# Kernel tuning notes

Measured on AMD Instinct MI355X. Metric: run time of the kernel, lower is better.

The kernel has to match this reference:

```python
import jax, jax.numpy as jnp
import numpy as np
from jax import lax

ALIGNED_H = 7
ALIGNED_W = 7
SPATIAL_SCALE = 0.125
B, C, H, W = 4, 512, 96, 96
R = 512
IMG = 768  # image resolution (features are image/8)


def setup_inputs() -> dict:
    key = jax.random.key(0)
    k1, k2, k3, k4, k5, k6 = jax.random.split(key, 6)
    features = jax.random.normal(k1, (B, C, H, W), dtype=jnp.float32)
    # realistic rois: [batch_idx, x1, y1, x2, y2] in image coordinates
    bi = jax.random.randint(k2, (R,), 0, B).astype(jnp.float32)
    cx = jax.random.uniform(k3, (R,), minval=32.0, maxval=float(IMG - 32))
    cy = jax.random.uniform(k4, (R,), minval=32.0, maxval=float(IMG - 32))
    bw = jax.random.uniform(k5, (R,), minval=16.0, maxval=256.0)
    bh = jax.random.uniform(k6, (R,), minval=16.0, maxval=256.0)
    x1 = jnp.clip(cx - bw / 2, 0.0, IMG - 1.0)
    x2 = jnp.clip(cx + bw / 2, 0.0, IMG - 1.0)
    y1 = jnp.clip(cy - bh / 2, 0.0, IMG - 1.0)
    y2 = jnp.clip(cy + bh / 2, 0.0, IMG - 1.0)
    rois = jnp.stack([bi, x1, y1, x2, y2], axis=1)
    return {"features": features, "rois": rois}


def _roi_align_ada(features, rois, ah, aw, scale):
    """RoIAlignAda: per output pixel, average of a 3x3 adaptive-stride grid of
    bilinear samples centered at the bin point (RT-MDNet ROIAlignAdaForward)."""
    b, c, h, w = features.shape
    r = rois.shape[0]
    batch_ind = rois[:, 0].astype(jnp.int32)
    x1 = rois[:, 1] * scale
    y1 = rois[:, 2] * scale
    x2 = rois[:, 3] * scale
    y2 = rois[:, 4] * scale
    roi_w = jnp.maximum(x2 - x1, 0.0)
    roi_h = jnp.maximum(y2 - y1, 0.0)
    bin_h = roi_h / (ah - 1.0)  # [R]
    bin_w = roi_w / (aw - 1.0)
    ph = jnp.arange(ah, dtype=jnp.float32)
    pw = jnp.arange(aw, dtype=jnp.float32)
    hc = y1[:, None] + ph[None, :] * bin_h[:, None]  # [R, AH] bin centers
    wc = x1[:, None] + pw[None, :] * bin_w[:, None]  # [R, AW]
    stride_h = jnp.maximum(1.0, jnp.round(bin_h / 3.0))  # [R]
    stride_w = jnp.maximum(1.0, jnp.round(bin_w / 3.0))

    center_ok = ((hc >= 0) & (hc < h))[:, :, None] & ((wc >= 0) & (wc < w))[:, None, :]  # [R,AH,AW]

    # flatten spatial for gathers: [B*H*W, C]
    f = features.transpose(0, 2, 3, 1).reshape(b * h * w, c)
    base = batch_ind[:, None, None] * (h * w)  # [R,1,1]

    acc = jnp.zeros((r, ah, aw, c), dtype=features.dtype)
    cnt = jnp.zeros((r, ah, aw), dtype=features.dtype)
    for sh in (-1.0, 0.0, 1.0):
        for sw in (-1.0, 0.0, 1.0):
            ch = hc + sh * stride_h[:, None]  # [R,AH]
            cw = wc + sw * stride_w[:, None]  # [R,AW]
            valid = ((ch >= 0) & (ch < h))[:, :, None] & ((cw >= 0) & (cw < w))[:, None, :]
            hs = jnp.clip(jnp.floor(ch), 0.0, h - 2.0)
            ws = jnp.clip(jnp.floor(cw), 0.0, w - 2.0)
            hr = (ch - hs)[:, :, None]  # [R,AH,1]
            wr = (cw - ws)[:, None, :] * jnp.ones((r, ah, aw), features.dtype)[:, :1, :1]  # broadcast helper
            wr = (cw - ws)[:, None, :]  # [R,1,AW]
            hsi = hs.astype(jnp.int32)[:, :, None]  # [R,AH,1]
            wsi = ws.astype(jnp.int32)[:, None, :]  # [R,1,AW]
            ul = base + hsi * w + wsi  # [R,AH,AW]
            v = (f[ul] * ((1.0 - hr) * (1.0 - wr))[..., None]
                 + f[ul + 1] * ((1.0 - hr) * wr)[..., None]
                 + f[ul + w] * (hr * (1.0 - wr))[..., None]
                 + f[ul + w + 1] * (hr * wr)[..., None])  # [R,AH,AW,C]
            acc = acc + jnp.where(valid[..., None], v, 0.0)
            cnt = cnt + valid.astype(features.dtype)

    out = jnp.where(center_ok[..., None], acc / jnp.maximum(cnt, 1.0)[..., None], 0.0)
    return out.transpose(0, 3, 1, 2)  # [R, C, AH, AW]


def reference(features, rois):
    x = _roi_align_ada(features, rois, ALIGNED_H + 4, ALIGNED_W + 4, SPATIAL_SCALE)  # [R,C,11,11]
    # fused 3x3 stride-2 max pool -> [R, C, 5, 5]
    out = lax.reduce_window(x, -jnp.inf, lax.max,
                            window_dimensions=(1, 1, 3, 3),
                            window_strides=(1, 1, 2, 2),
                            padding='VALID')
    return out
```

## Files before the change

### kernel.cpp

```cpp
#include <hip/hip_runtime.h>
#include <stdint.h>

typedef unsigned short u16;
typedef unsigned int   u32;

#define Bn 4
#define Cc 512
#define Hh 96
#define Ww 96
#define HWc (Hh*Ww)
#define AH 11
#define Rr 512
#define CP (Cc/2)

__device__ __forceinline__ u16 f2bf(float f){
  u32 u = __float_as_uint(f);
  u += 0x7fffu + ((u>>16)&1u);
  return (u16)(u>>16);
}
__device__ __forceinline__ u32 pk2(float a, float b){
  return (u32)f2bf(a) | ((u32)f2bf(b)<<16);
}

__global__ __launch_bounds__(256)
void transpose_kernel(const float* __restrict__ in, u32* __restrict__ out){
  __shared__ u32 tile[128*64];
  const int t = threadIdx.x;
  const int hw0 = blockIdx.x*128, c0 = blockIdx.y*128, b = blockIdx.z;
  {
    const int q = t & 31, cp0 = t >> 5;
    const float* ib = in + ((size_t)(b*Cc + c0))*HWc + hw0 + 4*q;
    #pragma unroll
    for (int p=0;p<8;++p){
      const int cp = cp0 + p*8;
      const float* pa = ib + (size_t)(2*cp)*HWc;
      float4 A = *(const float4*)pa;
      float4 B = *(const float4*)(pa + HWc);
      const int cs = cp ^ q;
      tile[(4*q+0)*64 + cs] = pk2(A.x,B.x);
      tile[(4*q+1)*64 + cs] = pk2(A.y,B.y);
      tile[(4*q+2)*64 + cs] = pk2(A.z,B.z);
      tile[(4*q+3)*64 + cs] = pk2(A.w,B.w);
    }
  }
  __syncthreads();
  {
    const int l = t & 63, wv = t >> 6;
    u32* ob = out + ((size_t)b*HWc + hw0)*CP + (c0>>1) + l;
    #pragma unroll
    for (int k=0;k<32;++k){
      const int hw = wv*32 + k;
      ob[(size_t)hw*CP] = tile[hw*64 + (l ^ (hw>>2))];
    }
  }
}

__global__ __launch_bounds__(128)
void roi_align_max_nhwc(const u32* __restrict__ feat,
                        const float* __restrict__ rois,
                        float* __restrict__ out)
{
  __shared__ __align__(16) int4   s_ro[AH];
  __shared__ __align__(16) float4 s_rw[AH];
  __shared__ __align__(16) int4   s_co[AH];
  __shared__ __align__(16) float4 s_cw[AH];
  __shared__ int s_b;
  __shared__ __align__(16) float s_out[256*25];

  const int t    = threadIdx.x;
  const int r    = blockIdx.x >> 1;
  const int half = blockIdx.x & 1;

  if (t == 0){
    int b = (int)rois[r*5+0];
    s_b = min(max(b, 0), Bn-1);
  }

  if (t < AH || (t >= 64 && t < 64+AH)){
    const bool isrow = (t < AH);
    const int  p = isrow ? t : t-64;
    const float* rp = rois + r*5;
    const float c1 = rp[isrow?2:1], c2 = rp[isrow?4:3];
    float lo  = __fmul_rn(c1, 0.125f);
    float hi  = __fmul_rn(c2, 0.125f);
    float ext = fmaxf(__fsub_rn(hi,lo), 0.0f);
    float bin = __fdiv_rn(ext, 10.0f);
    float ctr = __fadd_rn(lo, __fmul_rn((float)p, bin));
    float strd = fmaxf(1.0f, rintf(__fdiv_rn(bin, 3.0f)));
    bool ok = (ctr >= 0.0f) && (ctr < 96.0f);
    int rws[6]; float wts[6]; int nv=0;
    #pragma unroll
    for (int s=0;s<3;++s){
      float cc = __fadd_rn(ctr, __fmul_rn((float)(s-1), strd));
      bool vv = (cc >= 0.0f) && (cc < 96.0f);
      float fl = fminf(fmaxf(floorf(cc),0.0f),94.0f);
      float fr = __fsub_rn(cc, fl);
      int ri = (int)fl;
      rws[2*s]=ri; rws[2*s+1]=ri+1;
      wts[2*s]  = vv ? __fsub_rn(1.0f,fr) : 0.0f;
      wts[2*s+1]= vv ? fr : 0.0f;
      nv += vv?1:0;
    }
    float sc = ok ? (1.0f/(float)nv) : 0.0f;
    int cr[4]={0,0,0,0}; float cwv[4]={0.0f,0.0f,0.0f,0.0f}; int n=0;
    for (int k=0;k<6;++k){
      float wk=wts[k]; if (wk==0.0f) continue;
      int rr=rws[k]; bool fnd=false;
      for (int j=0;j<n;++j) if (cr[j]==rr){ cwv[j]+=wk; fnd=true; break; }
      if (!fnd && n<4){ cr[n]=rr; cwv[n]=wk; ++n; }
    }
    const int mul = isrow ? (Ww*CP) : CP;
    if (isrow){
      s_ro[p] = make_int4(cr[0]*mul, cr[1]*mul, cr[2]*mul, cr[3]*mul);
      s_rw[p] = make_float4(cwv[0]*sc, cwv[1]*sc, cwv[2]*sc, cwv[3]*sc);
    } else {
      s_co[p] = make_int4(cr[0]*mul, cr[1]*mul, cr[2]*mul, cr[3]*mul);
      s_cw[p] = make_float4(cwv[0]*sc, cwv[1]*sc, cwv[2]*sc, cwv[3]*sc);
    }
  }
  __syncthreads();

  const u32* fbase = feat + (size_t)s_b*((size_t)HWc*CP);
  const int tb = half*128 + t;

  int   vo[AH][4]; float cwr[AH][4];
  #pragma unroll
  for (int pw=0; pw<AH; ++pw){
    int4 c4 = s_co[pw]; float4 w4 = s_cw[pw];
    vo[pw][0]=tb+c4.x; vo[pw][1]=tb+c4.y; vo[pw][2]=tb+c4.z; vo[pw][3]=tb+c4.w;
    cwr[pw][0]=w4.x; cwr[pw][1]=w4.y; cwr[pw][2]=w4.z; cwr[pw][3]=w4.w;
  }

  float2 awin[5];
  #pragma unroll 1
  for (int ph=0; ph<AH; ++ph){
    int4   r4 = s_ro[ph];
    float4 w4 = s_rw[ph];
    const u32* r0 = fbase + __builtin_amdgcn_readfirstlane(r4.x);
    const u32* r1 = fbase + __builtin_amdgcn_readfirstlane(r4.y);
    const u32* r2 = fbase + __builtin_amdgcn_readfirstlane(r4.z);
    const u32* r3 = fbase + __builtin_amdgcn_readfirstlane(r4.w);
    const float rw_[4] = {w4.x, w4.y, w4.z, w4.w};
    float2 binr[AH];
    #pragma unroll
    for (int pw=0; pw<AH; ++pw){
      u32 v[16];
      #pragma unroll
      for (int j=0;j<4;++j){
        v[0*4+j] = r0[vo[pw][j]];
        v[1*4+j] = r1[vo[pw][j]];
        v[2*4+j] = r2[vo[pw][j]];
        v[3*4+j] = r3[vo[pw][j]];
      }
      float ax=0.0f, ay=0.0f;
      #pragma unroll
      for (int i=0;i<4;++i){
        float cx=0.0f, cy=0.0f;
        #pragma unroll
        for (int j=0;j<4;++j){
          u32 d = v[i*4+j];
          cx = fmaf(cwr[pw][j], __uint_as_float(d<<16),           cx);
          cy = fmaf(cwr[pw][j], __uint_as_float(d & 0xffff0000u), cy);
        }
        ax = fmaf(rw_[i], cx, ax);
        ay = fmaf(rw_[i], cy, ay);
      }
      binr[pw] = make_float2(ax, ay);
    }
    float2 rm[5];
    #pragma unroll
    for (int ox=0; ox<5; ++ox){
      rm[ox].x = fmaxf(fmaxf(binr[2*ox].x, binr[2*ox+1].x), binr[2*ox+2].x);
      rm[ox].y = fmaxf(fmaxf(binr[2*ox].y, binr[2*ox+1].y), binr[2*ox+2].y);
    }
    if (ph == 0){
      #pragma unroll
      for (int ox=0; ox<5; ++ox) awin[ox] = rm[ox];
    } else if (ph & 1){
      #pragma unroll
      for (int ox=0; ox<5; ++ox){
        awin[ox].x = fmaxf(awin[ox].x, rm[ox].x);
        awin[ox].y = fmaxf(awin[ox].y, rm[ox].y);
      }
    } else {
      const int oy = (ph-2) >> 1;
      #pragma unroll
      for (int ox=0; ox<5; ++ox){
        s_out[(2*t  )*25 + oy*5 + ox] = fmaxf(awin[ox].x, rm[ox].x);
        s_out[(2*t+1)*25 + oy*5 + ox] = fmaxf(awin[ox].y, rm[ox].y);
        awin[ox] = rm[ox];
      }
    }
  }
  __syncthreads();

  float4* dst = (float4*)(out + (size_t)r*(Cc*25) + half*(256*25));
  const float4* src = (const float4*)s_out;
  for (int k=t; k<(256*25)/4; k+=128) dst[k]=src[k];
}

__global__ __launch_bounds__(512, 1)
void roi_align_max_nchw(const float* __restrict__ feat,
                        const float* __restrict__ rois,
                        float* __restrict__ out)
{
  __shared__ int   s_roff[AH][6];
  __shared__ float s_rw  [AH][6];
  __shared__ int   s_coff[AH][6];
  __shared__ float s_cw  [AH][6];
  __shared__ int   s_b;
  __shared__ __align__(16) float s_out[Cc*25];

  const int t = threadIdx.x;
  const int r = blockIdx.x;

  if (t < AH*6){
    ((float*)s_rw)[t] = 0.0f;  ((int*)s_roff)[t] = 0;
    ((float*)s_cw)[t] = 0.0f;  ((int*)s_coff)[t] = 0;
  }
  if (t == 0){
    int b = (int)rois[r*5+0];
    s_b = min(max(b, 0), Bn-1);
  }
  __syncthreads();

  if (t < AH || (t >= 64 && t < 64+AH)){
    const bool isrow = (t < AH);
    const int  p = isrow ? t : t-64;
    const float* rp = rois + r*5;
    const float c1 = rp[isrow?2:1], c2 = rp[isrow?4:3];
    float lo  = __fmul_rn(c1, 0.125f);
    float hi  = __fmul_rn(c2, 0.125f);
    float ext = fmaxf(__fsub_rn(hi,lo), 0.0f);
    float bin = __fdiv_rn(ext, 10.0f);
    float ctr = __fadd_rn(lo, __fmul_rn((float)p, bin));
    float strd = fmaxf(1.0f, rintf(__fdiv_rn(bin, 3.0f)));
    bool ok = (ctr >= 0.0f) && (ctr < 96.0f);
    int rws[6]; float wts[6]; int nv=0;
    #pragma unroll
    for (int s=0;s<3;++s){
      float cc = __fadd_rn(ctr, __fmul_rn((float)(s-1), strd));
      bool vv = (cc >= 0.0f) && (cc < 96.0f);
      float fl = fminf(fmaxf(floorf(cc),0.0f),94.0f);
      float fr = __fsub_rn(cc, fl);
      int ri = (int)fl;
      rws[2*s]=ri; rws[2*s+1]=ri+1;
      wts[2*s]  = vv ? __fsub_rn(1.0f,fr) : 0.0f;
      wts[2*s+1]= vv ? fr : 0.0f;
      nv += vv?1:0;
    }
    float sc = ok ? (1.0f/(float)nv) : 0.0f;
    int cr[6]; float cw[6]; int n=0;
    for (int k=0;k<6;++k){
      float wk=wts[k]; if (wk==0.0f) continue;
      if (n>0 && cr[n-1]==rws[k]) cw[n-1]+=wk;
      else { cr[n]=rws[k]; cw[n]=wk; ++n; }
    }
    const int mul = isrow ? Ww : 1;
    for (int k=0;k<n;++k){
      int off = cr[k]*mul;
      float wv = cw[k]*sc;
      if (isrow){ s_roff[p][k]=off; s_rw[p][k]=wv; }
      else      { s_coff[p][k]=off; s_cw[p][k]=wv; }
    }
  }
  __syncthreads();

  const float* f0 = feat + ((size_t)s_b*Cc + t)*HWc;
  float awin[5];
  for (int ph=0; ph<AH; ++ph){
    float binrow[AH];
    #pragma unroll
    for (int pw=0; pw<AH; ++pw){
      float acc = 0.0f;
      #pragma unroll
      for (int ai=0; ai<6; ++ai){
        float ra = s_rw[ph][ai];
        if (ra == 0.0f) continue;
        int ro = s_roff[ph][ai];
        #pragma unroll
        for (int bi=0; bi<6; ++bi){
          float cb = s_cw[pw][bi];
          if (cb == 0.0f) continue;
          acc = fmaf(ra*cb, f0[ro + s_coff[pw][bi]], acc);
        }
      }
      binrow[pw] = acc;
    }
    float rm[5];
    #pragma unroll
    for (int ox=0; ox<5; ++ox)
      rm[ox] = fmaxf(fmaxf(binrow[2*ox], binrow[2*ox+1]), binrow[2*ox+2]);
    if (ph == 0){
      #pragma unroll
      for (int ox=0; ox<5; ++ox) awin[ox] = rm[ox];
    } else if (ph & 1){
      #pragma unroll
      for (int ox=0; ox<5; ++ox) awin[ox] = fmaxf(awin[ox], rm[ox]);
    } else {
      int oy = (ph-2) >> 1;
      #pragma unroll
      for (int ox=0; ox<5; ++ox){
        s_out[t*25 + oy*5 + ox] = fmaxf(awin[ox], rm[ox]);
        awin[ox] = rm[ox];
      }
    }
  }
  __syncthreads();

  float4* dst = (float4*)(out + (size_t)r*(Cc*25));
  const float4* src = (const float4*)s_out;
  for (int k=t; k<(Cc*25)/4; k+=512) dst[k]=src[k];
}

extern "C" void kernel_launch(void* const* d_in, const int* in_sizes, int n_in,
                              void* d_out, int out_size, void* d_ws, size_t ws_size,
                              hipStream_t stream)
{
  (void)in_sizes; (void)n_in; (void)out_size;
  const float* feat = (const float*)d_in[0];
  const float* rois = (const float*)d_in[1];
  float* out = (float*)d_out;
  const size_t need = (size_t)Bn*HWc*Cc*sizeof(u16);
  if (ws_size >= need){
    u32* ws = (u32*)d_ws;
    dim3 g(HWc/128, Cc/128, Bn);
    transpose_kernel<<<g, 256, 0, stream>>>(feat, ws);
    roi_align_max_nhwc<<<Rr*2, 128, 0, stream>>>(ws, rois, out);
  } else {
    roi_align_max_nchw<<<Rr, 512, 0, stream>>>(feat, rois, out);
  }
}
```

Before: 173.5 us.

## Split RoI align blocks into two row segments to double grid parallelism

```diff
diff --git a/kernel.cpp b/kernel.cpp
--- a/kernel.cpp
+++ b/kernel.cpp
@@ -55,6 +55,75 @@
   }
 }
 
+
+template<int NPH, int NOY>
+__device__ __forceinline__ void roi_seg_body(
+    const u32* __restrict__ fbase,
+    const int4* s_ro, const float4* s_rw,
+    const int (*vo)[4], const float (*cwr)[4],
+    float* __restrict__ s_out, int t, int LO)
+{
+  float2 awin[5];
+  #pragma unroll 1
+  for (int lp=0; lp<NPH; ++lp){
+    const int ph = LO + lp;
+    int4   r4 = s_ro[ph];
+    float4 w4 = s_rw[ph];
+    const u32* r0 = fbase + __builtin_amdgcn_readfirstlane(r4.x);
+    const u32* r1 = fbase + __builtin_amdgcn_readfirstlane(r4.y);
+    const u32* r2 = fbase + __builtin_amdgcn_readfirstlane(r4.z);
+    const u32* r3 = fbase + __builtin_amdgcn_readfirstlane(r4.w);
+    const float rw_[4] = {w4.x, w4.y, w4.z, w4.w};
+    float2 binr[AH];
+    #pragma unroll
+    for (int pw=0; pw<AH; ++pw){
+      u32 v[16];
+      #pragma unroll
+      for (int j=0;j<4;++j){
+        v[0*4+j] = r0[vo[pw][j]];
+        v[1*4+j] = r1[vo[pw][j]];
+        v[2*4+j] = r2[vo[pw][j]];
+        v[3*4+j] = r3[vo[pw][j]];
+      }
+      float ax=0.0f, ay=0.0f;
+      #pragma unroll
+      for (int i=0;i<4;++i)
+        #pragma unroll
+        for (int j=0;j<4;++j){
+          float w = rw_[i]*cwr[pw][j];
+          u32 d = v[i*4+j];
+          ax = fmaf(w, __uint_as_float(d<<16),           ax);
+          ay = fmaf(w, __uint_as_float(d & 0xffff0000u), ay);
+        }
+      binr[pw] = make_float2(ax, ay);
+    }
+    float2 rm[5];
+    #pragma unroll
+    for (int ox=0; ox<5; ++ox){
+      rm[ox].x = fmaxf(fmaxf(binr[2*ox].x, binr[2*ox+1].x), binr[2*ox+2].x);
+      rm[ox].y = fmaxf(fmaxf(binr[2*ox].y, binr[2*ox+1].y), binr[2*ox+2].y);
+    }
+    if (lp == 0){
+      #pragma unroll
+      for (int ox=0; ox<5; ++ox) awin[ox] = rm[ox];
+    } else if (lp & 1){
+      #pragma unroll
+      for (int ox=0; ox<5; ++ox){
+        awin[ox].x = fmaxf(awin[ox].x, rm[ox].x);
+        awin[ox].y = fmaxf(awin[ox].y, rm[ox].y);
+      }
+    } else {
+      const int ol = (lp-2) >> 1;
+      #pragma unroll
+      for (int ox=0; ox<5; ++ox){
+        s_out[(2*t  )*(NOY*5) + ol*5 + ox] = fmaxf(awin[ox].x, rm[ox].x);
+        s_out[(2*t+1)*(NOY*5) + ol*5 + ox] = fmaxf(awin[ox].y, rm[ox].y);
+        awin[ox] = rm[ox];
+      }
+    }
+  }
+}
+
 __global__ __launch_bounds__(128)
 void roi_align_max_nhwc(const u32* __restrict__ feat,
                         const float* __restrict__ rois,
@@ -65,11 +134,14 @@
   __shared__ __align__(16) int4   s_co[AH];
   __shared__ __align__(16) float4 s_cw[AH];
   __shared__ int s_b;
-  __shared__ __align__(16) float s_out[256*25];
+  __shared__ __align__(16) float s_out[256*15];
 
   const int t    = threadIdx.x;
-  const int r    = blockIdx.x >> 1;
-  const int half = blockIdx.x & 1;
+  const int bid  = blockIdx.x;
+  const int r    = bid & 511;
+  const int k    = bid >> 9;
+  const int half = k & 1;
+  const int seg  = k >> 1;
 
   if (t == 0){
     int b = (int)rois[r*5+0];
@@ -103,9 +175,9 @@
     }
     float sc = ok ? (1.0f/(float)nv) : 0.0f;
     int cr[4]={0,0,0,0}; float cwv[4]={0.0f,0.0f,0.0f,0.0f}; int n=0;
-    for (int k=0;k<6;++k){
-      float wk=wts[k]; if (wk==0.0f) continue;
-      int rr=rws[k]; bool fnd=false;
+    for (int kk=0;kk<6;++kk){
+      float wk=wts[kk]; if (wk==0.0f) continue;
+      int rr=rws[kk]; bool fnd=false;
       for (int j=0;j<n;++j) if (cr[j]==rr){ cwv[j]+=wk; fnd=true; break; }
       if (!fnd && n<4){ cr[n]=rr; cwv[n]=wk; ++n; }
     }
@@ -131,72 +203,16 @@
     cwr[pw][0]=w4.x; cwr[pw][1]=w4.y; cwr[pw][2]=w4.z; cwr[pw][3]=w4.w;
   }
 
-  float2 awin[5];
-  #pragma unroll 1
-  for (int ph=0; ph<AH; ++ph){
-    int4   r4 = s_ro[ph];
-    float4 w4 = s_rw[ph];
-    const u32* r0 = fbase + __builtin_amdgcn_readfirstlane(r4.x);
-    const u32* r1 = fbase + __builtin_amdgcn_readfirstlane(r4.y);
-    const u32* r2 = fbase + __builtin_amdgcn_readfirstlane(r4.z);
-    const u32* r3 = fbase + __builtin_amdgcn_readfirstlane(r4.w);
-    const float rw_[4] = {w4.x, w4.y, w4.z, w4.w};
-    float2 binr[AH];
-    #pragma unroll
-    for (int pw=0; pw<AH; ++pw){
-      u32 v[16];
-      #pragma unroll
-      for (int j=0;j<4;++j){
-        v[0*4+j] = r0[vo[pw][j]];
-        v[1*4+j] = r1[vo[pw][j]];
-        v[2*4+j] = r2[vo[pw][j]];
-        v[3*4+j] = r3[vo[pw][j]];
-      }
-      float ax=0.0f, ay=0.0f;
-      #pragma unroll
-      for (int i=0;i<4;++i){
-        float cx=0.0f, cy=0.0f;
-        #pragma unroll
-        for (int j=0;j<4;++j){
-          u32 d = v[i*4+j];
-          cx = fmaf(cwr[pw][j], __uint_as_float(d<<16),           cx);
-          cy = fmaf(cwr[pw][j], __uint_as_float(d & 0xffff0000u), cy);
-        }
-        ax = fmaf(rw_[i], cx, ax);
-        ay = fmaf(rw_[i], cy, ay);
-      }
-      binr[pw] = make_float2(ax, ay);
-    }
-    float2 rm[5];
-    #pragma unroll
-    for (int ox=0; ox<5; ++ox){
-      rm[ox].x = fmaxf(fmaxf(binr[2*ox].x, binr[2*ox+1].x), binr[2*ox+2].x);
-      rm[ox].y = fmaxf(fmaxf(binr[2*ox].y, binr[2*ox+1].y), binr[2*ox+2].y);
-    }
-    if (ph == 0){
-      #pragma unroll
-      for (int ox=0; ox<5; ++ox) awin[ox] = rm[ox];
-    } else if (ph & 1){
-      #pragma unroll
-      for (int ox=0; ox<5; ++ox){
-        awin[ox].x = fmaxf(awin[ox].x, rm[ox].x);
-        awin[ox].y = fmaxf(awin[ox].y, rm[ox].y);
-      }
-    } else {
-      const int oy = (ph-2) >> 1;
-      #pragma unroll
-      for (int ox=0; ox<5; ++ox){
-        s_out[(2*t  )*25 + oy*5 + ox] = fmaxf(awin[ox].x, rm[ox].x);
-        s_out[(2*t+1)*25 + oy*5 + ox] = fmaxf(awin[ox].y, rm[ox].y);
-        awin[ox] = rm[ox];
-      }
-    }
-  }
-  __syncthreads();
-
-  float4* dst = (float4*)(out + (size_t)r*(Cc*25) + half*(256*25));
-  const float4* src = (const float4*)s_out;
-  for (int k=t; k<(256*25)/4; k+=128) dst[k]=src[k];
+  if (seg == 0) roi_seg_body<5,2>(fbase, s_ro, s_rw, vo, cwr, s_out, t, 0);
+  else          roi_seg_body<7,3>(fbase, s_ro, s_rw, vo, cwr, s_out, t, 4);
+  __syncthreads();
+
+  const int noy5 = (seg==0) ? 10 : 15;
+  float* dst = out + (size_t)r*(Cc*25) + (size_t)half*(256*25) + (seg==0 ? 0 : 10);
+  for (int kk=t; kk<256*noy5; kk+=128){
+    int c = kk/noy5, j = kk - c*noy5;
+    dst[c*25 + j] = s_out[kk];
+  }
 }
 
 __global__ __launch_bounds__(512, 1)
@@ -251,17 +267,17 @@
     }
     float sc = ok ? (1.0f/(float)nv) : 0.0f;
     int cr[6]; float cw[6]; int n=0;
-    for (int k=0;k<6;++k){
-      float wk=wts[k]; if (wk==0.0f) continue;
-      if (n>0 && cr[n-1]==rws[k]) cw[n-1]+=wk;
-      else { cr[n]=rws[k]; cw[n]=wk; ++n; }
+    for (int kk=0;kk<6;++kk){
+      float wk=wts[kk]; if (wk==0.0f) continue;
+      if (n>0 && cr[n-1]==rws[kk]) cw[n-1]+=wk;
+      else { cr[n]=rws[kk]; cw[n]=wk; ++n; }
     }
     const int mul = isrow ? Ww : 1;
-    for (int k=0;k<n;++k){
-      int off = cr[k]*mul;
-      float wv = cw[k]*sc;
-      if (isrow){ s_roff[p][k]=off; s_rw[p][k]=wv; }
-      else      { s_coff[p][k]=off; s_cw[p][k]=wv; }
+    for (int kk=0;kk<n;++kk){
+      int off = cr[kk]*mul;
+      float wv = cw[kk]*sc;
+      if (isrow){ s_roff[p][kk]=off; s_rw[p][kk]=wv; }
+      else      { s_coff[p][kk]=off; s_cw[p][kk]=wv; }
     }
   }
   __syncthreads();
@@ -310,7 +326,7 @@
 
   float4* dst = (float4*)(out + (size_t)r*(Cc*25));
   const float4* src = (const float4*)s_out;
-  for (int k=t; k<(Cc*25)/4; k+=512) dst[k]=src[k];
+  for (int kk=t; kk<(Cc*25)/4; kk+=512) dst[kk]=src[kk];
 }
 
 extern "C" void kernel_launch(void* const* d_in, const int* in_sizes, int n_in,
@@ -326,7 +342,7 @@
     u32* ws = (u32*)d_ws;
     dim3 g(HWc/128, Cc/128, Bn);
     transpose_kernel<<<g, 256, 0, stream>>>(feat, ws);
-    roi_align_max_nhwc<<<Rr*2, 128, 0, stream>>>(ws, rois, out);
+    roi_align_max_nhwc<<<Rr*4, 128, 0, stream>>>(ws, rois, out);
   } else {
     roi_align_max_nchw<<<Rr, 512, 0, stream>>>(feat, rois, out);
   }
```

Result: slower. 220.7 us (+27.2%).
